# Kernel tuning notes

Measured on AMD Instinct MI355X. Metric: run time of the kernel, lower is better.

The kernel has to match this reference:

```python
import jax, jax.numpy as jnp
import numpy as np

N_EXPERTS = 64
TOP_K = 2
LOAD_BALANCE_COEF = 0.01
D_MODEL = 4096
N_TOKENS = 16384


def setup_inputs() -> dict:
    key = jax.random.key(0)
    kx, kw = jax.random.split(key)
    x = jax.random.normal(kx, (N_TOKENS, D_MODEL), dtype=jnp.float32)
    # nn.init.normal_(gate.weight, std=0.01); shape (n_experts, d_model)
    gate_w = 0.01 * jax.random.normal(kw, (N_EXPERTS, D_MODEL), dtype=jnp.float32)
    return {"x": x, "gate_w": gate_w}


def reference(x, gate_w):
    # logits: (N, n_experts)
    logits = jnp.einsum('nd,ed->ne', x, gate_w)
    router_probs = jax.nn.softmax(logits, axis=-1)
    top_k_weights, top_k_indices = jax.lax.top_k(router_probs, TOP_K)
    routing_weights = top_k_weights / jnp.sum(top_k_weights, axis=-1, keepdims=True)
    top1 = top_k_indices[:, 0]
    one_hot = jax.nn.one_hot(top1, N_EXPERTS, dtype=x.dtype)  # (N, n_experts)
    f_i = jnp.mean(one_hot, axis=0)          # fraction of tokens per expert (detached)
    p_i = jnp.mean(router_probs, axis=0)     # mean router prob per expert (diff.)
    load_balance_loss = LOAD_BALANCE_COEF * jnp.sum(jax.lax.stop_gradient(f_i) * p_i)
    return routing_weights, top_k_indices, load_balance_loss
```

## Files before the change

kernel.cpp:

```cpp
#include <hip/hip_runtime.h>
#include <math.h>

#define N_TOKENS 16384
#define D_MODEL  4096
#define N_EXP    64

#define TOKB  64
#define NWV   16
#define NSL   8
#define KSL   (D_MODEL / NSL)
#define CH    16
#define NCH   (KSL / CH)
#define PPAD  36
#define PFOFF (NWV * TOKB * PPAD)
#define NBLK  (N_TOKENS / TOKB)

__global__ void __launch_bounds__(256)
transpose_w(const float* __restrict__ w, float* __restrict__ wt) {
    __shared__ float t[64][65];
    const int k0 = blockIdx.x * 64;
    const int kc = (threadIdx.x & 15) * 4;
    const int e0 = threadIdx.x >> 4;
#pragma unroll
    for (int p = 0; p < 4; ++p) {
        int e = p * 16 + e0;
        float4 v = *(const float4*)(w + (size_t)e * D_MODEL + k0 + kc);
        t[kc + 0][e] = v.x; t[kc + 1][e] = v.y;
        t[kc + 2][e] = v.z; t[kc + 3][e] = v.w;
    }
    __syncthreads();
    const int kr = threadIdx.x >> 2;
    const int ec = (threadIdx.x & 3) * 16;
#pragma unroll
    for (int j = 0; j < 4; ++j) {
        float4 v = make_float4(t[kr][ec + j * 4 + 0], t[kr][ec + j * 4 + 1],
                               t[kr][ec + j * 4 + 2], t[kr][ec + j * 4 + 3]);
        *(float4*)(wt + (size_t)(k0 + kr) * N_EXP + ec + j * 4) = v;
    }
}

__global__ void __launch_bounds__(1024)
router_fused(const float* __restrict__ x, const float* __restrict__ wt,
             float* __restrict__ out, float* __restrict__ block_sums) {
    __shared__ float part[PFOFF + 2 * NWV * 64];

    const int tid  = threadIdx.x;
    const int wid  = tid >> 6;
    const int lane = tid & 63;
    const int tok0 = blockIdx.x * TOKB;

    const int wid_u = __builtin_amdgcn_readfirstlane(wid);
    const int h = wid_u & 1;
    const int s = wid_u >> 1;

    const float* xr = x + (size_t)(tok0 + lane) * D_MODEL + s * KSL;
    const float* wr = wt + (size_t)s * KSL * N_EXP + h * 32;

    float acc[32] = {};

#define K_STEP(wg, kidx, xv) do {                              \
        const float* wk_ = (wg) + (kidx) * N_EXP;              \
        const float xk_ = (xv);                                \
        _Pragma("unroll")                                      \
        for (int e = 0; e < 32; ++e)                           \
            acc[e] = fmaf(wk_[e], xk_, acc[e]);                \
    } while (0)

#define CHUNK_FMA(g, q0, q1, q2, q3) do {                      \
        const float* wg_ = wr + (size_t)(g) * CH * N_EXP;      \
        K_STEP(wg_,  0, (q0).x); K_STEP(wg_,  1, (q0).y);      \
        K_STEP(wg_,  2, (q0).z); K_STEP(wg_,  3, (q0).w);      \
        K_STEP(wg_,  4, (q1).x); K_STEP(wg_,  5, (q1).y);      \
        K_STEP(wg_,  6, (q1).z); K_STEP(wg_,  7, (q1).w);      \
        K_STEP(wg_,  8, (q2).x); K_STEP(wg_,  9, (q2).y);      \
        K_STEP(wg_, 10, (q2).z); K_STEP(wg_, 11, (q2).w);      \
        K_STEP(wg_, 12, (q3).x); K_STEP(wg_, 13, (q3).y);      \
        K_STEP(wg_, 14, (q3).z); K_STEP(wg_, 15, (q3).w);      \
    } while (0)

    float4 c0 = *(const float4*)(xr + 0);
    float4 c1 = *(const float4*)(xr + 4);
    float4 c2 = *(const float4*)(xr + 8);
    float4 c3 = *(const float4*)(xr + 12);

#pragma unroll 1
    for (int g = 0; g < NCH - 1; ++g) {
        const float* xn = xr + (size_t)(g + 1) * CH;
        float4 n0 = *(const float4*)(xn + 0);
        float4 n1 = *(const float4*)(xn + 4);
        float4 n2 = *(const float4*)(xn + 8);
        float4 n3 = *(const float4*)(xn + 12);

        __builtin_amdgcn_sched_barrier(0);

        CHUNK_FMA(g, c0, c1, c2, c3);

        c0 = n0; c1 = n1; c2 = n2; c3 = n3;
    }
    CHUNK_FMA(NCH - 1, c0, c1, c2, c3);

    {
        float* tp = part + (size_t)(wid * TOKB + lane) * PPAD;
#pragma unroll
        for (int e0 = 0; e0 < 32; e0 += 4)
            *(float4*)(tp + e0) = make_float4(acc[e0], acc[e0 + 1],
                                              acc[e0 + 2], acc[e0 + 3]);
    }
    __syncthreads();

    float p_acc = 0.f, f_acc = 0.f;
    const int he = lane >> 5;
    const int ew = lane & 31;
#pragma unroll 1
    for (int it = 0; it < 4; ++it) {
        const int tl = wid * 4 + it;
        float logit = 0.f;
#pragma unroll
        for (int sl = 0; sl < NSL; ++sl)
            logit += part[(size_t)((2 * sl + he) * TOKB + tl) * PPAD + ew];

        float m = logit;
#pragma unroll
        for (int off = 32; off; off >>= 1)
            m = fmaxf(m, __shfl_xor(m, off, 64));
        unsigned long long b1 = __ballot(logit == m);
        int i1 = __ffsll(b1) - 1;

        float p = expf(logit - m);
        float denom = p;
#pragma unroll
        for (int off = 32; off; off >>= 1)
            denom += __shfl_xor(denom, off, 64);

        p_acc += p / denom;
        if (lane == i1) f_acc += 1.f;

        float lx = (lane == i1) ? -__builtin_inff() : logit;
        float m2 = lx;
#pragma unroll
        for (int off = 32; off; off >>= 1)
            m2 = fmaxf(m2, __shfl_xor(m2, off, 64));
        unsigned long long b2 = __ballot(lx == m2);
        int i2 = __ffsll(b2) - 1;

        if (lane == 0) {
            float p1 = 1.0f / denom;
            float p2 = expf(m2 - m) / denom;
            float s12 = p1 + p2;
            int token = tok0 + tl;
            ((float2*)out)[token] = make_float2(p1 / s12, p2 / s12);
            ((float2*)(out + 2 * N_TOKENS))[token] =
                make_float2((float)i1, (float)i2);
        }
    }

    float* pf = part + PFOFF;
    pf[wid * 64 + lane]        = p_acc;
    pf[1024 + wid * 64 + lane] = f_acc;
    __syncthreads();
    if (tid < N_EXP) {
        float ps = 0.f, fs = 0.f;
#pragma unroll
        for (int hh = 0; hh < NWV; ++hh) {
            ps += pf[hh * 64 + tid];
            fs += pf[1024 + hh * 64 + tid];
        }
        block_sums[(size_t)blockIdx.x * 128 + tid]      = ps;
        block_sums[(size_t)blockIdx.x * 128 + 64 + tid] = fs;
    }
}

__global__ void __launch_bounds__(256)
router_final(const float* __restrict__ block_sums, float* __restrict__ out) {
    __shared__ float sp[4][N_EXP];
    __shared__ float sf[4][N_EXP];

    int tid  = threadIdx.x;
    int wv   = tid >> 6;
    int lane = tid & 63;

    float ps = 0.f, fs = 0.f;
#pragma unroll 8
    for (int b = wv * (NBLK / 4); b < (wv + 1) * (NBLK / 4); ++b) {
        ps += block_sums[(size_t)b * 128 + lane];
        fs += block_sums[(size_t)b * 128 + 64 + lane];
    }
    sp[wv][lane] = ps;
    sf[wv][lane] = fs;
    __syncthreads();

    if (tid < N_EXP) {
        float pt = sp[0][tid] + sp[1][tid] + sp[2][tid] + sp[3][tid];
        float ft = sf[0][tid] + sf[1][tid] + sf[2][tid] + sf[3][tid];
        float v = pt * ft;
#pragma unroll
        for (int off = 1; off < 64; off <<= 1)
            v += __shfl_xor(v, off, 64);
        if (tid == 0)
            out[4 * N_TOKENS] = 0.01f * v / ((float)N_TOKENS * (float)N_TOKENS);
    }
}

extern "C" void kernel_launch(void* const* d_in, const int* in_sizes, int n_in,
                              void* d_out, int out_size, void* d_ws, size_t ws_size,
                              hipStream_t stream) {
    (void)in_sizes; (void)n_in; (void)out_size; (void)ws_size;
    const float* x = (const float*)d_in[0];
    const float* w = (const float*)d_in[1];
    float* out = (float*)d_out;

    float* wT = (float*)d_ws;
    float* block_sums = wT + (size_t)D_MODEL * N_EXP;

    transpose_w<<<D_MODEL / 64, 256, 0, stream>>>(w, wT);
    router_fused<<<NBLK, 1024, 0, stream>>>(x, wT, out, block_sums);
    router_final<<<1, 256, 0, stream>>>(block_sums, out);
}
```

Measured before the change: 423.3 us.

## Stage x chunks through per-wave LDS transpose for coalesced global loads

Instead of each lane loading its own token's row with strided float4 loads, lanes now cooperatively load 16 tokens x 16 k-values per float4 group, which coalesces better. The data is transposed through a double-buffered per-wave LDS tile so each lane again holds its own token's 16 x values. This adds LDS write and read traffic on every chunk and reuses the partial-sum buffer region, so a barrier is added before that reuse. Launch bounds also now request 4 blocks, which may constrain register allocation for the 32 accumulators.

```diff
diff --git a/kernel.cpp b/kernel.cpp
--- a/kernel.cpp
+++ b/kernel.cpp
@@ -9,8 +9,11 @@
 #define NWV   16
 #define NSL   8
 #define KSL   (D_MODEL / NSL)
-#define CH    16
-#define NCH   (KSL / CH)
+#define CHK   16
+#define NCH   (KSL / CHK)
+#define XLD   68
+#define XTS   (CHK * XLD)
+#define WVS   (2 * XTS)
 #define PPAD  36
 #define PFOFF (NWV * TOKB * PPAD)
 #define NBLK  (N_TOKENS / TOKB)
@@ -39,10 +42,10 @@
     }
 }
 
-__global__ void __launch_bounds__(1024)
+__global__ void __launch_bounds__(1024, 4)
 router_fused(const float* __restrict__ x, const float* __restrict__ wt,
              float* __restrict__ out, float* __restrict__ block_sums) {
-    __shared__ float part[PFOFF + 2 * NWV * 64];
+    __shared__ float smem[PFOFF + 2 * NWV * 64];
 
     const int tid  = threadIdx.x;
     const int wid  = tid >> 6;
@@ -53,10 +56,49 @@
     const int h = wid_u & 1;
     const int s = wid_u >> 1;
 
-    const float* xr = x + (size_t)(tok0 + lane) * D_MODEL + s * KSL;
+    float* xtile = smem + wid * WVS;
+
+    const int sr = lane >> 2;
+    const int sq = lane & 3;
+
+    const float* xg = x + (size_t)(tok0 + sr) * D_MODEL + s * KSL + sq * 4;
     const float* wr = wt + (size_t)s * KSL * N_EXP + h * 32;
 
     float acc[32] = {};
+    float4 v0, v1, v2, v3;
+    float x0, x1, x2, x3, x4, x5, x6, x7, x8, x9, x10, x11, x12, x13, x14, x15;
+
+#define GLOAD(g) do {                                          \
+        const float* xp_ = xg + (size_t)(g) * CHK;             \
+        v0 = *(const float4*)(xp_);                            \
+        v1 = *(const float4*)(xp_ + (size_t)16 * D_MODEL);     \
+        v2 = *(const float4*)(xp_ + (size_t)32 * D_MODEL);     \
+        v3 = *(const float4*)(xp_ + (size_t)48 * D_MODEL);     \
+    } while (0)
+
+#define XWRITE(b) do {                                         \
+        float* t_ = xtile + (b) * XTS + (sq * 4) * XLD + sr;   \
+        t_[0 * XLD +  0] = v0.x; t_[1 * XLD +  0] = v0.y;      \
+        t_[2 * XLD +  0] = v0.z; t_[3 * XLD +  0] = v0.w;      \
+        t_[0 * XLD + 16] = v1.x; t_[1 * XLD + 16] = v1.y;      \
+        t_[2 * XLD + 16] = v1.z; t_[3 * XLD + 16] = v1.w;      \
+        t_[0 * XLD + 32] = v2.x; t_[1 * XLD + 32] = v2.y;      \
+        t_[2 * XLD + 32] = v2.z; t_[3 * XLD + 32] = v2.w;      \
+        t_[0 * XLD + 48] = v3.x; t_[1 * XLD + 48] = v3.y;      \
+        t_[2 * XLD + 48] = v3.z; t_[3 * XLD + 48] = v3.w;      \
+    } while (0)
+
+#define XREAD(b) do {                                          \
+        const float* t_ = xtile + (b) * XTS + lane;            \
+        x0  = t_[ 0 * XLD]; x1  = t_[ 1 * XLD];                \
+        x2  = t_[ 2 * XLD]; x3  = t_[ 3 * XLD];                \
+        x4  = t_[ 4 * XLD]; x5  = t_[ 5 * XLD];                \
+        x6  = t_[ 6 * XLD]; x7  = t_[ 7 * XLD];                \
+        x8  = t_[ 8 * XLD]; x9  = t_[ 9 * XLD];                \
+        x10 = t_[10 * XLD]; x11 = t_[11 * XLD];                \
+        x12 = t_[12 * XLD]; x13 = t_[13 * XLD];                \
+        x14 = t_[14 * XLD]; x15 = t_[15 * XLD];                \
+    } while (0)
 
 #define K_STEP(wg, kidx, xv) do {                              \
         const float* wk_ = (wg) + (kidx) * N_EXP;              \
@@ -66,41 +108,38 @@
             acc[e] = fmaf(wk_[e], xk_, acc[e]);                \
     } while (0)
 
-#define CHUNK_FMA(g, q0, q1, q2, q3) do {                      \
-        const float* wg_ = wr + (size_t)(g) * CH * N_EXP;      \
-        K_STEP(wg_,  0, (q0).x); K_STEP(wg_,  1, (q0).y);      \
-        K_STEP(wg_,  2, (q0).z); K_STEP(wg_,  3, (q0).w);      \
-        K_STEP(wg_,  4, (q1).x); K_STEP(wg_,  5, (q1).y);      \
-        K_STEP(wg_,  6, (q1).z); K_STEP(wg_,  7, (q1).w);      \
-        K_STEP(wg_,  8, (q2).x); K_STEP(wg_,  9, (q2).y);      \
-        K_STEP(wg_, 10, (q2).z); K_STEP(wg_, 11, (q2).w);      \
-        K_STEP(wg_, 12, (q3).x); K_STEP(wg_, 13, (q3).y);      \
-        K_STEP(wg_, 14, (q3).z); K_STEP(wg_, 15, (q3).w);      \
-    } while (0)
-
-    float4 c0 = *(const float4*)(xr + 0);
-    float4 c1 = *(const float4*)(xr + 4);
-    float4 c2 = *(const float4*)(xr + 8);
-    float4 c3 = *(const float4*)(xr + 12);
+#define CHUNK_FMA(g) do {                                      \
+        const float* wg_ = wr + (size_t)(g) * CHK * N_EXP;     \
+        K_STEP(wg_,  0, x0);  K_STEP(wg_,  1, x1);             \
+        K_STEP(wg_,  2, x2);  K_STEP(wg_,  3, x3);             \
+        K_STEP(wg_,  4, x4);  K_STEP(wg_,  5, x5);             \
+        K_STEP(wg_,  6, x6);  K_STEP(wg_,  7, x7);             \
+        K_STEP(wg_,  8, x8);  K_STEP(wg_,  9, x9);             \
+        K_STEP(wg_, 10, x10); K_STEP(wg_, 11, x11);            \
+        K_STEP(wg_, 12, x12); K_STEP(wg_, 13, x13);            \
+        K_STEP(wg_, 14, x14); K_STEP(wg_, 15, x15);            \
+    } while (0)
+
+    GLOAD(0);
+    XWRITE(0);
 
 #pragma unroll 1
     for (int g = 0; g < NCH - 1; ++g) {
-        const float* xn = xr + (size_t)(g + 1) * CH;
-        float4 n0 = *(const float4*)(xn + 0);
-        float4 n1 = *(const float4*)(xn + 4);
-        float4 n2 = *(const float4*)(xn + 8);
-        float4 n3 = *(const float4*)(xn + 12);
-
+        const int cur = g & 1;
+        const int nxt = cur ^ 1;
+
+        GLOAD(g + 1);
         __builtin_amdgcn_sched_barrier(0);
-
-        CHUNK_FMA(g, c0, c1, c2, c3);
-
-        c0 = n0; c1 = n1; c2 = n2; c3 = n3;
-    }
-    CHUNK_FMA(NCH - 1, c0, c1, c2, c3);
-
+        XREAD(cur);
+        CHUNK_FMA(g);
+        XWRITE(nxt);
+    }
+    XREAD((NCH - 1) & 1);
+    CHUNK_FMA(NCH - 1);
+
+    __syncthreads();
     {
-        float* tp = part + (size_t)(wid * TOKB + lane) * PPAD;
+        float* tp = smem + (size_t)(wid * TOKB + lane) * PPAD;
 #pragma unroll
         for (int e0 = 0; e0 < 32; e0 += 4)
             *(float4*)(tp + e0) = make_float4(acc[e0], acc[e0 + 1],
@@ -117,7 +156,7 @@
         float logit = 0.f;
 #pragma unroll
         for (int sl = 0; sl < NSL; ++sl)
-            logit += part[(size_t)((2 * sl + he) * TOKB + tl) * PPAD + ew];
+            logit += smem[(size_t)((2 * sl + he) * TOKB + tl) * PPAD + ew];
 
         float m = logit;
 #pragma unroll
@@ -154,7 +193,7 @@
         }
     }
 
-    float* pf = part + PFOFF;
+    float* pf = smem + PFOFF;
     pf[wid * 64 + lane]        = p_acc;
     pf[1024 + wid * 64 + lane] = f_acc;
     __syncthreads();
```

Measured after the change: 449.9 us. 6.3% more time.
